# Kernel optimization log

Hardware: AMD Instinct MI355X
Metric: run time of the kernel (lower is better)

## Reference

```python
import jax, jax.numpy as jnp
import numpy as np

B, N, D, H, L = 4, 1024, 256, 4, 2  # batch, nodes, mem_dim, heads, gcn sublayers
DK = D // H


def setup_inputs() -> dict:
    key = jax.random.key(0)
    ks = jax.random.split(key, 12)
    s = 0.05  # weight scale
    return {
        "gcn_inputs": jax.random.normal(ks[0], (B, N, D), jnp.float32),
        "rel_embs": jax.random.normal(ks[1], (B, N, D), jnp.float32),
        "adj": jax.random.randint(ks[2], (B, N, N), 0, 2, jnp.int32),
        "mask": jnp.zeros((B, 1, N), jnp.int32),  # 0 == valid token in this code's convention
        "W_Q": jax.random.normal(ks[3], (2 * D, D), jnp.float32) * s,
        "b_Q": jnp.zeros((D,), jnp.float32),
        "W_K": jax.random.normal(ks[4], (D, D), jnp.float32) * s,
        "b_K": jnp.zeros((D,), jnp.float32),
        "W_gcn": jax.random.normal(ks[5], (H * L, D, D), jnp.float32) * s,
        "b_gcn": jnp.zeros((H * L, D), jnp.float32),
        "W_out": jax.random.normal(ks[6], (D * H * L, D), jnp.float32) * s,
        "b_out": jnp.zeros((D,), jnp.float32),
    }


def _zscore_attn(scores, m, adj):
    """Faithful port of stdzscore + threshold + weightsoftmax chain.
    scores: [B,H,N,N]; m: bool [B,1,1,N] True=valid; adj: int [B,N,N]."""
    mf = m.astype(scores.dtype)
    # mymean (dim=[-1]): count from mask squeezed over dim -2 -> [B,1], +1e-4
    cnt_mean = mf[:, :, 0, :].sum(-1)[..., None] + 1e-4  # [B,1,1]
    ds = jnp.where(m, scores, 0.0).sum(-1)               # [B,H,N]
    mean = ds / cnt_mean                                  # [B,H,N]
    # mystd (dim=[-1]): count from full mask summed over -1 -> [B,1,1], +1e-4
    cnt_std = mf.sum(-1) + 1e-4                           # [B,1,1]
    sdata = jnp.where(m, (scores - mean[..., None]) ** 2, 0.0).sum(-1)
    std = jnp.sqrt(sdata / cnt_std + 1e-10)               # [B,H,N]
    z = (scores - mean[..., None]) / (std[..., None] + 1e-4)
    z = jnp.where(m, z, 0.0)
    thresh = z < 0
    s2 = jnp.where(thresh, -1e9, z)
    s2 = jnp.where(m, s2, -1e9)
    # weightsoftmax: stable exp, multiply by adjacency, mask, renormalize
    e = jnp.exp(s2 - s2.max(-1, keepdims=True))
    e = e * adj.astype(scores.dtype)[:, None]             # [B,H,N,N]
    e = jnp.where(m, e, 0.0) + 1e-10
    w = e / e.sum(-1, keepdims=True)
    w = jnp.where(m, w, 0.0)
    kill = (~m) | thresh | (adj == 0)[:, None]
    return jnp.where(kill, 0.0, w)


def reference(gcn_inputs, rel_embs, adj, mask, W_Q, b_Q, W_K, b_K, W_gcn, b_gcn, W_out, b_out):
    m = (mask == 0)[:, :, None, :]  # [B,1,1,N] True = valid
    # MultiHeadAttention: q from cat(query, rel), k from query
    q = (jnp.concatenate([gcn_inputs, rel_embs], -1) @ W_Q + b_Q)
    q = q.reshape(B, N, H, DK).transpose(0, 2, 1, 3)      # [B,H,N,DK]
    k = (gcn_inputs @ W_K + b_K).reshape(B, N, H, DK).transpose(0, 2, 1, 3)
    scores = jnp.einsum('bhnd,bhmd->bhnm', q, k)
    p_attn = _zscore_attn(scores, m, adj)                 # [B,H,N,N]
    # MultiGraphConvLayer (dropout = identity at inference)
    head_outs = []
    for i in range(H):
        a = p_attn[:, i]                                  # [B,N,N]
        denom = a.sum(2, keepdims=True) + 1.0             # [B,N,1]
        outputs = gcn_inputs
        layer_outs = []
        for l in range(L):
            idx = i * L + l
            Ax = jnp.einsum('bnm,bmd->bnd', a, outputs)
            # Linear applied to BOTH Ax and outputs (bias added twice, as in source)
            AxW = (Ax @ W_gcn[idx] + b_gcn[idx]) + (outputs @ W_gcn[idx] + b_gcn[idx])
            outputs = jax.nn.relu(AxW / denom)
            layer_outs.append(outputs)
        head_outs.append(jnp.concatenate(layer_outs, -1))  # [B,N,D*L]
    final = jnp.concatenate(head_outs, -1)                 # [B,N,D*L*H]
    return gcn_inputs + final @ W_out + b_out
```

## Files before the change

### kernel.cpp

```cpp
#include <hip/hip_runtime.h>
#include <math.h>

typedef unsigned short u16;
typedef __attribute__((ext_vector_type(8))) short short8;
typedef __attribute__((ext_vector_type(4))) float floatx4;

#define LDS_P 72

__device__ __forceinline__ float bf2f(u16 u) {
  union { unsigned int i; float f; } v; v.i = ((unsigned int)u) << 16; return v.f;
}
__device__ __forceinline__ u16 f2bf(float f) {
  union { float f; unsigned int i; } v; v.f = f;
  unsigned int x = v.i;
  return (u16)((x + 0x7FFFu + ((x >> 16) & 1u)) >> 16);
}

__device__ __forceinline__ void mfma_loop(const u16* __restrict__ A, int lda,
                                          const u16* __restrict__ Bt, int ldb,
                                          int K, u16* As, u16* Bs,
                                          floatx4 acc[2][2], int tid) {
  int lane = tid & 63;
  int wm = ((tid >> 6) & 1) << 5, wn = ((tid >> 6) >> 1) << 5;
  int lr = lane & 15, lq8 = (lane >> 4) << 3;
  int r0 = tid >> 3, c8 = (tid & 7) << 3;

  const u16* pA0 = A + (long long)r0 * lda + c8;
  const u16* pA1 = A + (long long)(r0 + 32) * lda + c8;
  const u16* pB0 = Bt + (long long)r0 * ldb + c8;
  const u16* pB1 = Bt + (long long)(r0 + 32) * ldb + c8;
  float4 a0 = *reinterpret_cast<const float4*>(pA0);
  float4 a1 = *reinterpret_cast<const float4*>(pA1);
  float4 b0 = *reinterpret_cast<const float4*>(pB0);
  float4 b1 = *reinterpret_cast<const float4*>(pB1);
  *reinterpret_cast<float4*>(As + r0 * LDS_P + c8) = a0;
  *reinterpret_cast<float4*>(As + (r0 + 32) * LDS_P + c8) = a1;
  *reinterpret_cast<float4*>(Bs + r0 * LDS_P + c8) = b0;
  *reinterpret_cast<float4*>(Bs + (r0 + 32) * LDS_P + c8) = b1;
  __syncthreads();

  int nslab = K >> 6;
  for (int s = 0; s < nslab; ++s) {
    const u16* Ac = As + (s & 1) * 4608;
    const u16* Bc = Bs + (s & 1) * 4608;
    if (s + 1 < nslab) {
      int off = (s + 1) << 6;
      a0 = *reinterpret_cast<const float4*>(pA0 + off);
      a1 = *reinterpret_cast<const float4*>(pA1 + off);
      b0 = *reinterpret_cast<const float4*>(pB0 + off);
      b1 = *reinterpret_cast<const float4*>(pB1 + off);
    }
#pragma unroll
    for (int kc = 0; kc < 64; kc += 32) {
      short8 fa0 = *reinterpret_cast<const short8*>(Ac + (wm + lr) * LDS_P + kc + lq8);
      short8 fa1 = *reinterpret_cast<const short8*>(Ac + (wm + 16 + lr) * LDS_P + kc + lq8);
      short8 fb0 = *reinterpret_cast<const short8*>(Bc + (wn + lr) * LDS_P + kc + lq8);
      short8 fb1 = *reinterpret_cast<const short8*>(Bc + (wn + 16 + lr) * LDS_P + kc + lq8);
      acc[0][0] = __builtin_amdgcn_mfma_f32_16x16x32_bf16(fa0, fb0, acc[0][0], 0, 0, 0);
      acc[0][1] = __builtin_amdgcn_mfma_f32_16x16x32_bf16(fa0, fb1, acc[0][1], 0, 0, 0);
      acc[1][0] = __builtin_amdgcn_mfma_f32_16x16x32_bf16(fa1, fb0, acc[1][0], 0, 0, 0);
      acc[1][1] = __builtin_amdgcn_mfma_f32_16x16x32_bf16(fa1, fb1, acc[1][1], 0, 0, 0);
    }
    if (s + 1 < nslab) {
      u16* An = As + ((s + 1) & 1) * 4608;
      u16* Bn = Bs + ((s + 1) & 1) * 4608;
      *reinterpret_cast<float4*>(An + r0 * LDS_P + c8) = a0;
      *reinterpret_cast<float4*>(An + (r0 + 32) * LDS_P + c8) = a1;
      *reinterpret_cast<float4*>(Bn + r0 * LDS_P + c8) = b0;
      *reinterpret_cast<float4*>(Bn + (r0 + 32) * LDS_P + c8) = b1;
    }
    __syncthreads();
  }
}

#define EPI_SETUP                                                     \
  int lane = threadIdx.x & 63;                                        \
  int wm = ((threadIdx.x >> 6) & 1) << 5,                             \
      wn = ((threadIdx.x >> 6) >> 1) << 5;                            \
  int lr = lane & 15, lq4 = (lane >> 4) << 2;

__global__ __launch_bounds__(256) void proj2_k(
    const u16* __restrict__ A, const u16* __restrict__ WQT,
    const u16* __restrict__ WKT, const float* __restrict__ b_Q,
    const float* __restrict__ b_K, u16* __restrict__ qbf,
    u16* __restrict__ kbf) {
  __shared__ u16 As[2 * 64 * LDS_P], Bs[2 * 64 * LDS_P];
  int z = blockIdx.z;
  int m0 = blockIdx.y << 6, n0 = blockIdx.x << 6;
  int K = z ? 256 : 512, ldb = z ? 256 : 512;
  const u16* Bt = z ? WKT : WQT;
  const float* bias = z ? b_K : b_Q;
  u16* C = z ? kbf : qbf;
  floatx4 acc[2][2] = {};
  mfma_loop(A + (long long)m0 * 512, 512, Bt + (long long)n0 * ldb, ldb, K, As, Bs,
            acc, threadIdx.x);
  EPI_SETUP
#pragma unroll
  for (int ti = 0; ti < 2; ++ti)
#pragma unroll
    for (int tj = 0; tj < 2; ++tj)
#pragma unroll
      for (int r = 0; r < 4; ++r) {
        int row = m0 + wm + ti * 16 + lq4 + r;
        int col = n0 + wn + tj * 16 + lr;
        C[(long long)row * 256 + col] = f2bf(acc[ti][tj][r] + bias[col]);
      }
}

__global__ __launch_bounds__(256) void mscore_k(
    const u16* __restrict__ q, const u16* __restrict__ kb,
    u16* __restrict__ sc) {
  __shared__ u16 As[2 * 64 * LDS_P], Bs[2 * 64 * LDS_P];
  int z = blockIdx.z;
  int b = z & 3, h = z >> 2;
  int m0 = blockIdx.y << 6, n0 = blockIdx.x << 6;
  const u16* Ab = q + b * 262144 + h * 64;
  const u16* Bb = kb + b * 262144 + h * 64;
  floatx4 acc[2][2] = {};
  mfma_loop(Ab + (long long)m0 * 256, 256, Bb + (long long)n0 * 256, 256, 64, As, Bs,
            acc, threadIdx.x);
  u16* Cb = sc + ((long long)z << 20);
  EPI_SETUP
#pragma unroll
  for (int ti = 0; ti < 2; ++ti)
#pragma unroll
    for (int tj = 0; tj < 2; ++tj)
#pragma unroll
      for (int r = 0; r < 4; ++r) {
        int row = m0 + wm + ti * 16 + lq4 + r;
        int col = n0 + wn + tj * 16 + lr;
        Cb[(long long)row * 1024 + col] = f2bf(acc[ti][tj][r]);
      }
}

__device__ __forceinline__ float wred_sum(float v) {
#pragma unroll
  for (int m = 32; m > 0; m >>= 1) v += __shfl_xor(v, m, 64);
  return v;
}
__device__ __forceinline__ void wred_sum2(float& a, float& b) {
#pragma unroll
  for (int m = 32; m > 0; m >>= 1) {
    float ta = __shfl_xor(a, m, 64);
    float tb = __shfl_xor(b, m, 64);
    a += ta; b += tb;
  }
}
__device__ __forceinline__ float wred_max(float v) {
#pragma unroll
  for (int m = 32; m > 0; m >>= 1) v = fmaxf(v, __shfl_xor(v, m, 64));
  return v;
}

__global__ __launch_bounds__(256) void zscore_w(
    const u16* __restrict__ sc, const int* __restrict__ adj,
    const int* __restrict__ mask, u16* __restrict__ wout,
    float* __restrict__ denh) {
  int wv = threadIdx.x >> 6, lane = threadIdx.x & 63;
  int row = (blockIdx.x << 2) + wv;
  int b = row >> 10, n = row & 1023;
  int e0 = lane << 4;
  const int* arow = adj + ((long long)row << 10) + e0;
  const int* mrow = mask + (b << 10) + e0;

  unsigned int vbits = 0, abits = 0;
#pragma unroll
  for (int q = 0; q < 4; ++q) {
    int4 a4 = *reinterpret_cast<const int4*>(arow + (q << 2));
    int4 m4 = *reinterpret_cast<const int4*>(mrow + (q << 2));
    vbits |= (unsigned)(m4.x == 0) << (q * 4);
    vbits |= (unsigned)(m4.y == 0) << (q * 4 + 1);
    vbits |= (unsigned)(m4.z == 0) << (q * 4 + 2);
    vbits |= (unsigned)(m4.w == 0) << (q * 4 + 3);
    abits |= (unsigned)(a4.x != 0) << (q * 4);
    abits |= (unsigned)(a4.y != 0) << (q * 4 + 1);
    abits |= (unsigned)(a4.z != 0) << (q * 4 + 2);
    abits |= (unsigned)(a4.w != 0) << (q * 4 + 3);
  }
  float cnt = wred_sum((float)__popc(vbits));
  float cnteff = cnt + 0.0001f;

  for (int h = 0; h < 4; ++h) {
    int z = (h << 2) + b;
    const u16* srow = sc + ((long long)z << 20) + ((long long)n << 10) + e0;
    float s[16];
#pragma unroll
    for (int q = 0; q < 2; ++q) {
      uint4 u = *reinterpret_cast<const uint4*>(srow + (q << 3));
      unsigned int uu[4] = {u.x, u.y, u.z, u.w};
#pragma unroll
      for (int t = 0; t < 4; ++t) {
        union { unsigned int i; float f; } lo, hi;
        lo.i = uu[t] << 16;
        hi.i = uu[t] & 0xffff0000u;
        s[q * 8 + t * 2] = lo.f;
        s[q * 8 + t * 2 + 1] = hi.f;
      }
    }
    float suml = 0.f, sql = 0.f;
#pragma unroll
    for (int u = 0; u < 16; ++u)
      if ((vbits >> u) & 1) { suml += s[u]; sql += s[u] * s[u]; }
    wred_sum2(suml, sql);
    float mean = suml / cnteff;
    float sdata = sql - 2.f * mean * suml + cnt * mean * mean;
    float stdv = sqrtf(fmaxf(sdata, 0.f) / cnteff + 1e-10f);
    float inv = 1.f / (stdv + 0.0001f);

    float maxl = -1e9f;
#pragma unroll
    for (int u = 0; u < 16; ++u) {
      float zz = (s[u] - mean) * inv;
      int vv = (vbits >> u) & 1;
      zz = vv ? zz : 0.f;
      s[u] = zz;
      if (vv && zz >= 0.f) maxl = fmaxf(maxl, zz);
    }
    float rowmax = wred_max(maxl);

    float e[16], el = 0.f;
#pragma unroll
    for (int u = 0; u < 16; ++u) {
      int vv = (vbits >> u) & 1, aa = (abits >> u) & 1;
      float ev = (vv && aa && (s[u] >= 0.f)) ? expf(s[u] - rowmax) : 0.f;
      e[u] = ev + 1e-10f;
      el += e[u];
    }
    float esum = wred_sum(el);
    float rinv = 1.f / esum;

    float wl = 0.f;
    unsigned int wo[8];
#pragma unroll
    for (int u = 0; u < 16; u += 2) {
      int s0 = ((vbits >> u) & 1) && ((abits >> u) & 1) && (s[u] >= 0.f);
      int s1 = ((vbits >> (u + 1)) & 1) && ((abits >> (u + 1)) & 1) && (s[u + 1] >= 0.f);
      float w0 = s0 ? e[u] * rinv : 0.f;
      float w1 = s1 ? e[u + 1] * rinv : 0.f;
      wl += w0 + w1;
      wo[u >> 1] = (unsigned)f2bf(w0) | ((unsigned)f2bf(w1) << 16);
    }
    float wsum = wred_sum(wl);

    u16* orow = wout + ((size_t)z << 20) + ((size_t)n << 10) + e0;
    reinterpret_cast<uint4*>(orow)[0] = make_uint4(wo[0], wo[1], wo[2], wo[3]);
    reinterpret_cast<uint4*>(orow)[1] = make_uint4(wo[4], wo[5], wo[6], wo[7]);
    if (lane == 0) denh[(z << 10) + n] = wsum + 1.0f;
  }
}

__global__ __launch_bounds__(512) void gcn_k(
    const u16* __restrict__ wght, const u16* __restrict__ srcT, int zmaskB,
    const u16* __restrict__ addsrc, int ldadd, long long sAdd, int hmul,
    const u16* __restrict__ WgT_all, const float* __restrict__ bg_all,
    const float* __restrict__ den, int l,
    u16* __restrict__ obT, u16* __restrict__ fin) {
  __shared__ u16 lds[53760];
  u16* As0 = lds;
  u16* As1 = lds + 4608;
  u16* Bs0 = lds + 9216;
  u16* Bs1 = lds + 27648;
  u16* Ts = lds;
  u16* Ws0 = lds + 16896;
  u16* Ws1 = lds + 35328;
  int tid = threadIdx.x;
  int m0 = blockIdx.x << 6;
  int z = blockIdx.y;
  int lane = tid & 63, w = tid >> 6;
  int wm = (w & 1) << 5, wn = (w >> 1) << 6;
  int lr = lane & 15, lq8 = (lane >> 4) << 3, lq4 = (lane >> 4) << 2;

  const u16* Aw = wght + ((long long)z << 20) + (long long)m0 * 1024;
  const u16* Bt = srcT + (long long)(z & zmaskB) * 262144;
  const u16* addb = addsrc + (long long)(z & 3) * sAdd + (z >> 2) * hmul;
  int idx2 = (z >> 2) * 2 + l;
  const u16* Wg = WgT_all + (long long)idx2 * 65536;

  floatx4 acc[2][4] = {};
  int rA = tid >> 3, cA = (tid & 7) << 3;
  int rowB[4], colB[4];
#pragma unroll
  for (int j = 0; j < 4; ++j) {
    int id = tid + (j << 9);
    rowB[j] = id >> 3; colB[j] = (id & 7) << 3;
  }

  float4 pa, pb[4];
  pa = *reinterpret_cast<const float4*>(Aw + (long long)rA * 1024 + cA);
#pragma unroll
  for (int j = 0; j < 4; ++j)
    pb[j] = *reinterpret_cast<const float4*>(Bt + (long long)rowB[j] * 1024 + colB[j]);
  *reinterpret_cast<float4*>(As0 + rA * 72 + cA) = pa;
#pragma unroll
  for (int j = 0; j < 4; ++j)
    *reinterpret_cast<float4*>(Bs0 + rowB[j] * 72 + colB[j]) = pb[j];
  __syncthreads();

  for (int s = 0; s < 16; ++s) {
    const u16* Ac = (s & 1) ? As1 : As0;
    const u16* Bc = (s & 1) ? Bs1 : Bs0;
    if (s < 15) {
      int off = (s + 1) << 6;
      pa = *reinterpret_cast<const float4*>(Aw + (long long)rA * 1024 + off + cA);
#pragma unroll
      for (int j = 0; j < 4; ++j)
        pb[j] = *reinterpret_cast<const float4*>(Bt + (long long)rowB[j] * 1024 + off + colB[j]);
    }
#pragma unroll
    for (int kc = 0; kc < 64; kc += 32) {
      short8 a[2], b[4];
#pragma unroll
      for (int t = 0; t < 2; ++t)
        a[t] = *reinterpret_cast<const short8*>(Ac + (wm + t * 16 + lr) * 72 + kc + lq8);
#pragma unroll
      for (int t = 0; t < 4; ++t)
        b[t] = *reinterpret_cast<const short8*>(Bc + (wn + t * 16 + lr) * 72 + kc + lq8);
#pragma unroll
      for (int ti = 0; ti < 2; ++ti)
#pragma unroll
        for (int tj = 0; tj < 4; ++tj)
          acc[ti][tj] =
              __builtin_amdgcn_mfma_f32_16x16x32_bf16(a[ti], b[tj], acc[ti][tj], 0, 0, 0);
    }
    if (s < 15) {
      u16* An = (s & 1) ? As0 : As1;
      u16* Bn = (s & 1) ? Bs0 : Bs1;
      *reinterpret_cast<float4*>(An + rA * 72 + cA) = pa;
#pragma unroll
      for (int j = 0; j < 4; ++j)
        *reinterpret_cast<float4*>(Bn + rowB[j] * 72 + colB[j]) = pb[j];
    }
    __syncthreads();
  }

#pragma unroll
  for (int ti = 0; ti < 2; ++ti)
#pragma unroll
    for (int tj = 0; tj < 4; ++tj)
#pragma unroll
      for (int r = 0; r < 4; ++r) {
        int row = wm + ti * 16 + lq4 + r;
        int col = wn + tj * 16 + lr;
        float v = acc[ti][tj][r] + bf2f(addb[(long long)(m0 + row) * ldadd + col]);
        Ts[row * 264 + col] = f2bf(v);
        acc[ti][tj][r] = 0.f;
      }
  float4 pw[4];
#pragma unroll
  for (int j = 0; j < 4; ++j)
    pw[j] = *reinterpret_cast<const float4*>(Wg + (long long)rowB[j] * 256 + colB[j]);
#pragma unroll
  for (int j = 0; j < 4; ++j)
    *reinterpret_cast<float4*>(Ws0 + rowB[j] * 72 + colB[j]) = pw[j];
  __syncthreads();

  for (int s = 0; s < 4; ++s) {
    const u16* Wc = (s & 1) ? Ws1 : Ws0;
    int kc0 = s << 6;
    if (s < 3) {
      int off = (s + 1) << 6;
#pragma unroll
      for (int j = 0; j < 4; ++j)
        pw[j] = *reinterpret_cast<const float4*>(Wg + (long long)rowB[j] * 256 + off + colB[j]);
    }
#pragma unroll
    for (int kc = 0; kc < 64; kc += 32) {
      short8 a[2], b[4];
#pragma unroll
      for (int t = 0; t < 2; ++t)
        a[t] = *reinterpret_cast<const short8*>(Ts + (wm + t * 16 + lr) * 264 + kc0 + kc + lq8);
#pragma unroll
      for (int t = 0; t < 4; ++t)
        b[t] = *reinterpret_cast<const short8*>(Wc + (wn + t * 16 + lr) * 72 + kc + lq8);
#pragma unroll
      for (int ti = 0; ti < 2; ++ti)
#pragma unroll
        for (int tj = 0; tj < 4; ++tj)
          acc[ti][tj] =
              __builtin_amdgcn_mfma_f32_16x16x32_bf16(a[ti], b[tj], acc[ti][tj], 0, 0, 0);
    }
    if (s < 3) {
      u16* Wn = (s & 1) ? Ws0 : Ws1;
#pragma unroll
      for (int j = 0; j < 4; ++j)
        *reinterpret_cast<float4*>(Wn + rowB[j] * 72 + colB[j]) = pw[j];
    }
    __syncthreads();
  }

  const float* bb = bg_all + idx2 * 256;
  const float* dn = den + (z << 10);
  long long finbase = (long long)(z & 3) * 2097152 + idx2 * 256;
#pragma unroll
  for (int ti = 0; ti < 2; ++ti) {
    int row = m0 + wm + ti * 16 + lq4;
#pragma unroll
    for (int tj = 0; tj < 4; ++tj) {
      int col = wn + tj * 16 + lr;
      u16 bv4[4];
#pragma unroll
      for (int r = 0; r < 4; ++r) {
        float v = (acc[ti][tj][r] + 2.f * bb[col]) / dn[row + r];
        v = fmaxf(v, 0.f);
        bv4[r] = f2bf(v);
        fin[finbase + (long long)(row + r) * 2048 + col] = bv4[r];
      }
      if (obT) {
        ushort4 t4 = {bv4[0], bv4[1], bv4[2], bv4[3]};
        *reinterpret_cast<ushort4*>(obT + ((long long)z << 18) +
                                    (long long)col * 1024 + row) = t4;
      }
    }
  }
}

__global__ __launch_bounds__(256) void mfinal_k(
    const u16* __restrict__ fin, const u16* __restrict__ WoT,
    float* __restrict__ out) {
  __shared__ u16 As[2 * 64 * LDS_P], Bs[2 * 64 * LDS_P];
  int m0 = blockIdx.y << 6, n0 = blockIdx.x << 6;
  int ks = blockIdx.z << 9;
  floatx4 acc[2][2] = {};
  mfma_loop(fin + (long long)m0 * 2048 + ks, 2048, WoT + (long long)n0 * 2048 + ks,
            2048, 512, As, Bs, acc, threadIdx.x);
  EPI_SETUP
#pragma unroll
  for (int ti = 0; ti < 2; ++ti)
#pragma unroll
    for (int tj = 0; tj < 2; ++tj)
#pragma unroll
      for (int r = 0; r < 4; ++r) {
        int row = m0 + wm + ti * 16 + lq4 + r;
        int col = n0 + wn + tj * 16 + lr;
        atomicAdd(out + (long long)row * 256 + col, acc[ti][tj][r]);
      }
}

__global__ __launch_bounds__(256) void prep_k(
    const float* __restrict__ X, const float* __restrict__ R,
    const float* __restrict__ W_Q, const float* __restrict__ W_K,
    const float* __restrict__ W_gcn, const float* __restrict__ W_out,
    const float* __restrict__ b_out,
    u16* __restrict__ A, u16* __restrict__ XT, u16* __restrict__ WQT,
    u16* __restrict__ WKT, u16* __restrict__ WgT, u16* __restrict__ WoT,
    float* __restrict__ out) {
  int bi = blockIdx.x;
  int tid = threadIdx.x;
  if (bi < 560) {
    __shared__ u16 tile[64 * LDS_P];
    const float* S;
    u16* D;
    int I, ti, tj;
    if (bi < 256) {
      int zz = bi >> 6, rem = bi & 63;
      ti = rem >> 2; tj = rem & 3; I = 1024;
      S = X + zz * 262144; D = XT + zz * 262144;
    } else if (bi < 288) {
      int t = bi - 256; ti = t >> 2; tj = t & 3; I = 512;
      S = W_Q; D = WQT;
    } else if (bi < 304) {
      int t = bi - 288; ti = t >> 2; tj = t & 3; I = 256;
      S = W_K; D = WKT;
    } else if (bi < 432) {
      int t = bi - 304; int zz = t >> 4, rem = t & 15;
      ti = rem >> 2; tj = rem & 3; I = 256;
      S = W_gcn + zz * 65536; D = WgT + zz * 65536;
    } else {
      int t = bi - 432; ti = t >> 2; tj = t & 3; I = 2048;
      S = W_out; D = WoT;
    }
    int rr = tid >> 4, cc = (tid & 15) << 2;
#pragma unroll
    for (int q = 0; q < 4; ++q) {
      int r = rr + (q << 4);
      float4 v = *reinterpret_cast<const float4*>(S + (long long)(ti * 64 + r) * 256 +
                                                  tj * 64 + cc);
      ushort4 h = {f2bf(v.x), f2bf(v.y), f2bf(v.z), f2bf(v.w)};
      *reinterpret_cast<ushort4*>(tile + r * LDS_P + cc) = h;
    }
    __syncthreads();
    int jl = tid >> 2, il = (tid & 3) << 4;
    u16 vals[16];
#pragma unroll
    for (int u = 0; u < 16; ++u) vals[u] = tile[(il + u) * LDS_P + jl];
    u16* dp = D + (long long)(tj * 64 + jl) * I + ti * 64 + il;
    reinterpret_cast<uint4*>(dp)[0] = *reinterpret_cast<uint4*>(vals);
    reinterpret_cast<uint4*>(dp)[1] = *reinterpret_cast<uint4*>(vals + 8);
  } else if (bi < 8752) {
    int gid = (bi - 560) * 256 + tid;
    int col = gid & 511, row = gid >> 9;
    float v = (col < 256) ? X[row * 256 + col] : R[row * 256 + col - 256];
    A[gid] = f2bf(v);
  } else {
    int t = (bi - 8752) * 256 + tid;
    int col = (t << 2) & 255;
    float4 x = reinterpret_cast<const float4*>(X)[t];
    float4 b = *reinterpret_cast<const float4*>(b_out + col);
    x.x += b.x; x.y += b.y; x.z += b.z; x.w += b.w;
    reinterpret_cast<float4*>(out)[t] = x;
  }
}

extern "C" void kernel_launch(void* const* d_in, const int* in_sizes, int n_in,
                              void* d_out, int out_size, void* d_ws, size_t ws_size,
                              hipStream_t stream) {
  const float* X = (const float*)d_in[0];
  const float* R = (const float*)d_in[1];
  const int* adj = (const int*)d_in[2];
  const int* mask = (const int*)d_in[3];
  const float* W_Q = (const float*)d_in[4];
  const float* b_Q = (const float*)d_in[5];
  const float* W_K = (const float*)d_in[6];
  const float* b_K = (const float*)d_in[7];
  const float* W_gcn = (const float*)d_in[8];
  const float* b_gcn = (const float*)d_in[9];
  const float* W_out = (const float*)d_in[10];
  const float* b_out = (const float*)d_in[11];
  float* out = (float*)d_out;

  u16* wsu = (u16*)d_ws;
  u16* A_qk = wsu;
  u16* qbf  = A_qk + (2u << 20);
  u16* kbf  = qbf + (1u << 20);
  u16* XT   = kbf + (1u << 20);
  u16* WQT  = XT + (1u << 20);
  u16* WKT  = WQT + (1u << 17);
  u16* WgT  = WKT + (1u << 16);
  u16* WoT  = WgT + (1u << 19);
  u16* obT  = WoT + (1u << 19);
  u16* finb = obT + (4u << 20);
  u16* wght = finb + (8u << 20);
  float* den = (float*)(wght + (16u << 20));
  u16* sc = (u16*)(den + (1 << 14));

  prep_k<<<9776, 256, 0, stream>>>(X, R, W_Q, W_K, W_gcn, W_out, b_out,
                                   A_qk, XT, WQT, WKT, WgT, WoT, out);

  proj2_k<<<dim3(4, 64, 2), 256, 0, stream>>>(A_qk, WQT, WKT, b_Q, b_K, qbf, kbf);

  mscore_k<<<dim3(16, 16, 16), 256, 0, stream>>>(qbf, kbf, sc);
  zscore_w<<<1024, 256, 0, stream>>>(sc, adj, mask, wght, den);

  gcn_k<<<dim3(16, 16), 512, 0, stream>>>(wght, XT, 3, A_qk, 512, 524288LL, 0,
                                          WgT, b_gcn, den, 0, obT, finb);
  gcn_k<<<dim3(16, 16), 512, 0, stream>>>(wght, obT, 15, finb, 2048, 2097152LL, 512,
                                          WgT, b_gcn, den, 1, nullptr, finb);

  mfinal_k<<<dim3(4, 64, 4), 256, 0, stream>>>(finb, WoT, out);
}
```

Before: 212.7 us.

## Replace split-K atomic final GEMM with full-K double-buffered kernel and fused residual

The final output projection no longer splits K four ways with float atomics. Each 512-thread block now computes a 64x64 output tile over the full 2048-long K loop, using register-prefetched double-buffered LDS tiles and 16x16x32 bf16 MFMA. The residual plus bias initialisation moves out of prep_k into this kernel's epilogue, so atomics and the separate out-initialisation pass go away. In exchange the grid shrinks to 256 blocks, each running a longer serial K loop, which may leave the GPU under-occupied.

```diff
diff --git a/kernel.cpp b/kernel.cpp
--- a/kernel.cpp
+++ b/kernel.cpp
@@ -414,36 +414,74 @@
   }
 }
 
-__global__ __launch_bounds__(256) void mfinal_k(
+__global__ __launch_bounds__(512) void mfinal_k(
     const u16* __restrict__ fin, const u16* __restrict__ WoT,
+    const float* __restrict__ X, const float* __restrict__ bias,
     float* __restrict__ out) {
-  __shared__ u16 As[2 * 64 * LDS_P], Bs[2 * 64 * LDS_P];
+  __shared__ u16 lds[36864];
+  u16* As0 = lds;
+  u16* As1 = lds + 4608;
+  u16* Bs0 = lds + 9216;
+  u16* Bs1 = lds + 13824;
+  int tid = threadIdx.x;
   int m0 = blockIdx.y << 6, n0 = blockIdx.x << 6;
-  int ks = blockIdx.z << 9;
-  floatx4 acc[2][2] = {};
-  mfma_loop(fin + (long long)m0 * 2048 + ks, 2048, WoT + (long long)n0 * 2048 + ks,
-            2048, 512, As, Bs, acc, threadIdx.x);
-  EPI_SETUP
-#pragma unroll
-  for (int ti = 0; ti < 2; ++ti)
-#pragma unroll
-    for (int tj = 0; tj < 2; ++tj)
-#pragma unroll
-      for (int r = 0; r < 4; ++r) {
-        int row = m0 + wm + ti * 16 + lq4 + r;
-        int col = n0 + wn + tj * 16 + lr;
-        atomicAdd(out + (long long)row * 256 + col, acc[ti][tj][r]);
-      }
+  int lane = tid & 63, w = tid >> 6;
+  int wm = (w & 3) << 4, wn = (w >> 2) << 5;
+  int lr = lane & 15, lq8 = (lane >> 4) << 3, lq4 = (lane >> 4) << 2;
+
+  const u16* Ab = fin + (long long)m0 * 2048;
+  const u16* Bb = WoT + (long long)n0 * 2048;
+  int r0 = tid >> 3, c8 = (tid & 7) << 3;
+
+  floatx4 acc[2] = {};
+  float4 pa = *reinterpret_cast<const float4*>(Ab + (long long)r0 * 2048 + c8);
+  float4 pb = *reinterpret_cast<const float4*>(Bb + (long long)r0 * 2048 + c8);
+  *reinterpret_cast<float4*>(As0 + r0 * 72 + c8) = pa;
+  *reinterpret_cast<float4*>(Bs0 + r0 * 72 + c8) = pb;
+  __syncthreads();
+
+  for (int s = 0; s < 32; ++s) {
+    const u16* Ac = (s & 1) ? As1 : As0;
+    const u16* Bc = (s & 1) ? Bs1 : Bs0;
+    if (s < 31) {
+      int off = (s + 1) << 6;
+      pa = *reinterpret_cast<const float4*>(Ab + (long long)r0 * 2048 + off + c8);
+      pb = *reinterpret_cast<const float4*>(Bb + (long long)r0 * 2048 + off + c8);
+    }
+#pragma unroll
+    for (int kc = 0; kc < 64; kc += 32) {
+      short8 a = *reinterpret_cast<const short8*>(Ac + (wm + lr) * 72 + kc + lq8);
+      short8 b0 = *reinterpret_cast<const short8*>(Bc + (wn + lr) * 72 + kc + lq8);
+      short8 b1 = *reinterpret_cast<const short8*>(Bc + (wn + 16 + lr) * 72 + kc + lq8);
+      acc[0] = __builtin_amdgcn_mfma_f32_16x16x32_bf16(a, b0, acc[0], 0, 0, 0);
+      acc[1] = __builtin_amdgcn_mfma_f32_16x16x32_bf16(a, b1, acc[1], 0, 0, 0);
+    }
+    if (s < 31) {
+      u16* An = (s & 1) ? As0 : As1;
+      u16* Bn = (s & 1) ? Bs0 : Bs1;
+      *reinterpret_cast<float4*>(An + r0 * 72 + c8) = pa;
+      *reinterpret_cast<float4*>(Bn + r0 * 72 + c8) = pb;
+    }
+    __syncthreads();
+  }
+
+#pragma unroll
+  for (int tj = 0; tj < 2; ++tj)
+#pragma unroll
+    for (int r = 0; r < 4; ++r) {
+      int row = m0 + wm + lq4 + r;
+      int col = n0 + wn + tj * 16 + lr;
+      out[(long long)row * 256 + col] =
+          acc[tj][r] + bias[col] + X[(long long)row * 256 + col];
+    }
 }
 
 __global__ __launch_bounds__(256) void prep_k(
     const float* __restrict__ X, const float* __restrict__ R,
     const float* __restrict__ W_Q, const float* __restrict__ W_K,
     const float* __restrict__ W_gcn, const float* __restrict__ W_out,
-    const float* __restrict__ b_out,
     u16* __restrict__ A, u16* __restrict__ XT, u16* __restrict__ WQT,
-    u16* __restrict__ WKT, u16* __restrict__ WgT, u16* __restrict__ WoT,
-    float* __restrict__ out) {
+    u16* __restrict__ WKT, u16* __restrict__ WgT, u16* __restrict__ WoT) {
   int bi = blockIdx.x;
   int tid = threadIdx.x;
   if (bi < 560) {
@@ -486,18 +524,11 @@
     u16* dp = D + (long long)(tj * 64 + jl) * I + ti * 64 + il;
     reinterpret_cast<uint4*>(dp)[0] = *reinterpret_cast<uint4*>(vals);
     reinterpret_cast<uint4*>(dp)[1] = *reinterpret_cast<uint4*>(vals + 8);
-  } else if (bi < 8752) {
+  } else {
     int gid = (bi - 560) * 256 + tid;
     int col = gid & 511, row = gid >> 9;
     float v = (col < 256) ? X[row * 256 + col] : R[row * 256 + col - 256];
     A[gid] = f2bf(v);
-  } else {
-    int t = (bi - 8752) * 256 + tid;
-    int col = (t << 2) & 255;
-    float4 x = reinterpret_cast<const float4*>(X)[t];
-    float4 b = *reinterpret_cast<const float4*>(b_out + col);
-    x.x += b.x; x.y += b.y; x.z += b.z; x.w += b.w;
-    reinterpret_cast<float4*>(out)[t] = x;
   }
 }
 
@@ -533,8 +564,8 @@
   float* den = (float*)(wght + (16u << 20));
   u16* sc = (u16*)(den + (1 << 14));
 
-  prep_k<<<9776, 256, 0, stream>>>(X, R, W_Q, W_K, W_gcn, W_out, b_out,
-                                   A_qk, XT, WQT, WKT, WgT, WoT, out);
+  prep_k<<<8752, 256, 0, stream>>>(X, R, W_Q, W_K, W_gcn, W_out,
+                                   A_qk, XT, WQT, WKT, WgT, WoT);
 
   proj2_k<<<dim3(4, 64, 2), 256, 0, stream>>>(A_qk, WQT, WKT, b_Q, b_K, qbf, kbf);
 
@@ -546,5 +577,5 @@
   gcn_k<<<dim3(16, 16), 512, 0, stream>>>(wght, obT, 15, finb, 2048, 2097152LL, 512,
                                           WgT, b_gcn, den, 1, nullptr, finb);
 
-  mfinal_k<<<dim3(4, 64, 4), 256, 0, stream>>>(finb, WoT, out);
-}
+  mfinal_k<<<dim3(4, 64), 512, 0, stream>>>(finb, WoT, X, b_out, out);
+}
```

Measured after the change: 210.9 us. No clear change (-0.9%).
